# Kernel optimization log

Hardware: AMD Instinct MI355X
Metric: run time of the kernel (lower is better)

Reference implementation:

```python
import jax, jax.numpy as jnp
from jax import lax
import numpy as np

T, IN, H, L = 8192, 128, 1024, 3


def setup_inputs() -> dict:
    key = jax.random.key(0)
    ks = jax.random.split(key, 12)
    s = 0.05  # scale params to avoid saturating sigmoid/tanh
    return {
        "S": jax.random.normal(ks[0], (T, IN), jnp.float32),
        "h0": jax.random.normal(ks[1], (L, H), jnp.float32),
        "w_ih0": jax.random.normal(ks[2], (2 * H, IN), jnp.float32) * s,
        "w_hh0": jax.random.normal(ks[3], (2 * H, H), jnp.float32) * s,
        "b_ih0": jax.random.normal(ks[4], (2 * H,), jnp.float32) * s,
        "b_hh0": jax.random.normal(ks[5], (2 * H,), jnp.float32) * s,
        "w_ih_rest": jax.random.normal(ks[6], (L - 1, 2 * H, H), jnp.float32) * s,
        "w_hh_rest": jax.random.normal(ks[7], (L - 1, 2 * H, H), jnp.float32) * s,
        "b_ih_rest": jax.random.normal(ks[8], (L - 1, 2 * H), jnp.float32) * s,
        "b_hh_rest": jax.random.normal(ks[9], (L - 1, 2 * H), jnp.float32) * s,
        "w_out": jax.random.normal(ks[10], (1, H), jnp.float32) * s,
        "b_out": jax.random.normal(ks[11], (1,), jnp.float32) * s,
    }


def _mgu_layer(x_seq, h0, w_ih, w_hh, b_ih, b_hh):
    # Precompute the input projection for all timesteps at once: [T, 2H]
    gi = x_seq @ w_ih.T + b_ih

    def step(h, gi_t):
        gh = h @ w_hh.T + b_hh                      # [2H]
        i_f, i_n = jnp.split(gi_t, 2)
        h_f, h_n = jnp.split(gh, 2)
        f = jax.nn.sigmoid(i_f + h_f)               # forget gate
        n = jnp.tanh(i_n + f * h_n)                 # new candidate
        hy = n + (1.0 - f) * (h - n)
        return hy, hy

    _, out = lax.scan(step, h0, gi)                 # out: [T, H]
    return out


def reference(S, h0, w_ih0, w_hh0, b_ih0, b_hh0,
              w_ih_rest, w_hh_rest, b_ih_rest, b_hh_rest,
              w_out, b_out):
    x = _mgu_layer(S, h0[0], w_ih0, w_hh0, b_ih0, b_hh0)
    for l in range(w_ih_rest.shape[0]):             # fixed small layer count
        x = _mgu_layer(x, h0[l + 1], w_ih_rest[l], w_hh_rest[l],
                       b_ih_rest[l], b_hh_rest[l])
    out = (x @ w_out.T + b_out).reshape(-1)          # [T]
    return out
```

## Files before the change

### kernel.cpp

```cpp
#include <hip/hip_runtime.h>
#include <math.h>
#include <stdint.h>


#define T_STEPS 8192
#define HDIM 1024
#define RING 128

typedef unsigned long long u64;
typedef int v4i __attribute__((ext_vector_type(4)));

__device__ __forceinline__ u64 agload64(const u64* p) {
    return __hip_atomic_load(p, __ATOMIC_RELAXED, __HIP_MEMORY_SCOPE_AGENT);
}
__device__ __forceinline__ void agstore64(u64* p, u64 v) {
    __hip_atomic_store(p, v, __ATOMIC_RELAXED, __HIP_MEMORY_SCOPE_AGENT);
}
__device__ __forceinline__ int agloadi(const int* p) {
    return __hip_atomic_load(p, __ATOMIC_RELAXED, __HIP_MEMORY_SCOPE_AGENT);
}
__device__ __forceinline__ void agstorei(int* p, int v) {
    __hip_atomic_store(p, v, __ATOMIC_RELAXED, __HIP_MEMORY_SCOPE_AGENT);
}
__device__ __forceinline__ v4i poll16(const u64* p) {
    v4i r;
    asm volatile("global_load_dwordx4 %0, %1, off sc0 sc1\n\t"
                 "s_waitcnt vmcnt(0)"
                 : "=v"(r) : "v"(p) : "memory");
    return r;
}
__device__ __forceinline__ float dot4(float4 a, float4 b) {
    return a.x * b.x + a.y * b.y + a.z * b.z + a.w * b.w;
}
__device__ __forceinline__ u64 pack(float v, int tag) {
    return ((u64)(unsigned)tag << 32) | (u64)__float_as_uint(v);
}
__device__ __forceinline__ void opaque4(float4& v) {
    asm volatile("" : "+v"(v.x), "+v"(v.y), "+v"(v.z), "+v"(v.w));
}
__device__ __forceinline__ void opaque2(float2& v) {
    asm volatile("" : "+v"(v.x), "+v"(v.y));
}

template <int K, int L>
__device__ void scan_layer(float* __restrict__ s_h,
                           float* __restrict__ s_x,
                           const float* __restrict__ S,
                           const u64*  __restrict__ xring_in,
                           u64*        __restrict__ xring_out,
                           float*      __restrict__ xout,
                           const float* __restrict__ h0,
                           const float* __restrict__ w_ih,
                           const float* __restrict__ b_ih,
                           const float* __restrict__ w_hh,
                           const float* __restrict__ b_hh,
                           u64* __restrict__ htag,
                           int* __restrict__ progNext,
                           int* __restrict__ progSelf,
                           int r)
{
    const int tid = threadIdx.x;
    const int a   = tid >> 6;
    const int q   = tid & 63;
    const int jb  = r * 16 + 2 * a;

    float4 wf[2][4], wn[2][4];
#pragma unroll
    for (int g = 0; g < 2; ++g) {
        const float* rf = w_hh + (size_t)(jb + g) * HDIM;
        const float* rn = w_hh + (size_t)(HDIM + jb + g) * HDIM;
#pragma unroll
        for (int m = 0; m < 4; ++m) {
            wf[g][m] = *(const float4*)(rf + 4 * q + 256 * m);
            wn[g][m] = *(const float4*)(rn + 4 * q + 256 * m);
            opaque4(wf[g][m]); opaque4(wn[g][m]);
        }
    }
    float4 wif[2][4], win[2][4];
    float2 wif2[2], win2[2];
    if constexpr (K == 1024) {
#pragma unroll
        for (int g = 0; g < 2; ++g) {
            const float* rf = w_ih + (size_t)(jb + g) * K;
            const float* rn = w_ih + (size_t)(HDIM + jb + g) * K;
#pragma unroll
            for (int m = 0; m < 4; ++m) {
                wif[g][m] = *(const float4*)(rf + 4 * q + 256 * m);
                win[g][m] = *(const float4*)(rn + 4 * q + 256 * m);
                opaque4(wif[g][m]); opaque4(win[g][m]);
            }
        }
    } else {
#pragma unroll
        for (int g = 0; g < 2; ++g) {
            wif2[g] = *(const float2*)(w_ih + (size_t)(jb + g) * K + 2 * q);
            win2[g] = *(const float2*)(w_ih + (size_t)(HDIM + jb + g) * K + 2 * q);
            opaque2(wif2[g]); opaque2(win2[g]);
        }
    }
    float bFv[2], bInv[2], bHnv[2];
#pragma unroll
    for (int g = 0; g < 2; ++g) {
        bFv[g]  = b_ih[jb + g] + b_hh[jb + g];
        bInv[g] = b_ih[HDIM + jb + g];
        bHnv[g] = b_hh[HDIM + jb + g];
    }

    int lastProg = 0;
    for (int t = 0; t < T_STEPS; ++t) {
        const int par = t & 1;
        const u64* hrow = htag + (size_t)((t + 1) & 1) * HDIM;
        u64*       hpub = htag + (size_t)par * HDIM;
        float* hD = s_h + par * HDIM;
        float* xD = s_x + par * HDIM;

        if constexpr (L < 2) {
            if (t - lastProg > RING - 16) {
                do { lastProg = agloadi(progNext); } while (t - lastProg > RING - 16);
            }
        }

        if constexpr (L > 0) {
            const u64* xrow = xring_in + (size_t)(t & (RING - 1)) * HDIM;
            const unsigned xe = (unsigned)(t + 1);
            for (;;) {
                const v4i v = poll16(xrow + 2 * tid);
                if ((unsigned)v.y == xe && (unsigned)v.w == xe) {
                    ((float2*)xD)[tid] =
                        make_float2(__int_as_float(v.x), __int_as_float(v.z));
                    break;
                }
                __builtin_amdgcn_s_sleep(1);
            }
        } else {
            if (tid < K / 4)
                ((float4*)xD)[tid] = ((const float4*)(S + (size_t)t * K))[tid];
        }

        if (t == 0) {
            ((float2*)hD)[tid] = ((const float2*)h0)[tid];
        } else {
            const unsigned he = (unsigned)t;
            for (;;) {
                const v4i v = poll16(hrow + 2 * tid);
                if ((unsigned)v.y == he && (unsigned)v.w == he) {
                    ((float2*)hD)[tid] =
                        make_float2(__int_as_float(v.x), __int_as_float(v.z));
                    break;
                }
                __builtin_amdgcn_s_sleep(1);
            }
        }
        __syncthreads();

        if constexpr (L > 0) {
            if (r == 0 && tid == 0) agstorei(progSelf, t + 1);
        }

        float aF[2]  = {0.f, 0.f};
        float aNh[2] = {0.f, 0.f};
        float aNi[2] = {0.f, 0.f};
#pragma unroll
        for (int m = 0; m < 4; ++m) {
            const float4 h4 = ((const float4*)hD)[q + 64 * m];
#pragma unroll
            for (int g = 0; g < 2; ++g) {
                aF[g]  += dot4(wf[g][m], h4);
                aNh[g] += dot4(wn[g][m], h4);
            }
        }
        if constexpr (K == 1024) {
#pragma unroll
            for (int m = 0; m < 4; ++m) {
                const float4 x4 = ((const float4*)xD)[q + 64 * m];
#pragma unroll
                for (int g = 0; g < 2; ++g) {
                    aF[g]  += dot4(wif[g][m], x4);
                    aNi[g] += dot4(win[g][m], x4);
                }
            }
        } else {
            const float2 x2 = *(const float2*)&xD[2 * q];
#pragma unroll
            for (int g = 0; g < 2; ++g) {
                aF[g]  += wif2[g].x * x2.x + wif2[g].y * x2.y;
                aNi[g] += win2[g].x * x2.x + win2[g].y * x2.y;
            }
        }

#pragma unroll
        for (int g = 0; g < 2; ++g) {
            aF[g]  += __shfl_xor(aF[g],  1, 64);
            aNh[g] += __shfl_xor(aNh[g], 1, 64);
            aNi[g] += __shfl_xor(aNi[g], 1, 64);
        }
        const int gs = q & 1;
        float vF  = gs ? aF[1]  : aF[0];
        float vNh = gs ? aNh[1] : aNh[0];
        float vNi = gs ? aNi[1] : aNi[0];
#pragma unroll
        for (int off = 2; off <= 32; off <<= 1) {
            vF  += __shfl_xor(vF,  off, 64);
            vNh += __shfl_xor(vNh, off, 64);
            vNi += __shfl_xor(vNi, off, 64);
        }

        if (q < 2) {
            const float cF  = gs ? bFv[1]  : bFv[0];
            const float cIn = gs ? bInv[1] : bInv[0];
            const float cHn = gs ? bHnv[1] : bHnv[0];
            const int   j   = jb + q;
            const float hp  = hD[j];
            const float f   = 1.f / (1.f + expf(-(vF + cF)));
            const float n   = tanhf(vNi + cIn + f * (vNh + cHn));
            const float hy  = n + (1.f - f) * (hp - n);
            const u64   pk  = pack(hy, t + 1);
            agstore64(hpub + j, pk);
            if constexpr (L < 2) {
                agstore64(xring_out + (size_t)(t & (RING - 1)) * HDIM + j, pk);
            } else {
                xout[(size_t)t * HDIM + j] = hy;
            }
        }
    }
}

__global__ __launch_bounds__(512, 2)
void mgu_pipe(const float* __restrict__ S,
              const float* __restrict__ h0,
              const float* __restrict__ w_ih0, const float* __restrict__ b_ih0,
              const float* __restrict__ w_hh0, const float* __restrict__ b_hh0,
              const float* __restrict__ w_ih_r, const float* __restrict__ b_ih_r,
              const float* __restrict__ w_hh_r, const float* __restrict__ b_hh_r,
              float* __restrict__ xbuf2, u64* __restrict__ ring0,
              u64* __restrict__ ring1, u64* __restrict__ htag,
              int* __restrict__ prog)
{
    __shared__ __align__(16) float s_h[2 * HDIM];
    __shared__ __align__(16) float s_x[2 * HDIM];
    const int grp = blockIdx.x >> 6;
    const int r   = blockIdx.x & 63;
    if (grp == 0) {
        scan_layer<128, 0>(s_h, s_x, S, nullptr, ring0, nullptr, h0,
                           w_ih0, b_ih0, w_hh0, b_hh0,
                           htag, prog + 1, nullptr, r);
    } else if (grp == 1) {
        scan_layer<1024, 1>(s_h, s_x, nullptr, ring0, ring1, nullptr, h0 + HDIM,
                            w_ih_r, b_ih_r, w_hh_r, b_hh_r,
                            htag + 2 * HDIM, prog + 2, prog + 1, r);
    } else {
        scan_layer<1024, 2>(s_h, s_x, nullptr, ring1, nullptr, xbuf2,
                            h0 + 2 * HDIM,
                            w_ih_r + 2048 * 1024, b_ih_r + 2048,
                            w_hh_r + 2048 * 1024, b_hh_r + 2048,
                            htag + 4 * HDIM, nullptr, prog + 2, r);
    }
}

__global__ __launch_bounds__(256)
void mgu_out(const float* __restrict__ x,
             const float* __restrict__ w_out,
             const float* __restrict__ b_out,
             float* __restrict__ out)
{
    const int wave = threadIdx.x >> 6;
    const int lane = threadIdx.x & 63;
    const int t = blockIdx.x * 4 + wave;
    float acc = 0.f;
#pragma unroll
    for (int m = 0; m < 4; ++m) {
        const int i4 = lane + 64 * m;
        const float4 x4 = ((const float4*)(x + (size_t)t * HDIM))[i4];
        const float4 w4 = ((const float4*)w_out)[i4];
        acc += dot4(x4, w4);
    }
#pragma unroll
    for (int off = 32; off > 0; off >>= 1) acc += __shfl_xor(acc, off, 64);
    if (lane == 0) out[t] = acc + b_out[0];
}

extern "C" void kernel_launch(void* const* d_in, const int* in_sizes, int n_in,
                              void* d_out, int out_size, void* d_ws, size_t ws_size,
                              hipStream_t stream) {
    const float* S      = (const float*)d_in[0];
    const float* h0     = (const float*)d_in[1];
    const float* w_ih0  = (const float*)d_in[2];
    const float* w_hh0  = (const float*)d_in[3];
    const float* b_ih0  = (const float*)d_in[4];
    const float* b_hh0  = (const float*)d_in[5];
    const float* w_ih_r = (const float*)d_in[6];
    const float* w_hh_r = (const float*)d_in[7];
    const float* b_ih_r = (const float*)d_in[8];
    const float* b_hh_r = (const float*)d_in[9];
    const float* w_out  = (const float*)d_in[10];
    const float* b_out  = (const float*)d_in[11];
    float* out = (float*)d_out;

    char* ws = (char*)d_ws;
    float* xbuf2 = (float*)(ws);
    u64*   ring0 = (u64*)(ws + (32u << 20));
    u64*   ring1 = (u64*)(ws + (33u << 20));
    u64*   htag  = (u64*)(ws + (34u << 20));
    int*   prog  = (int*)(ws + (34u << 20) + (64u << 10));

    mgu_pipe<<<192, 512, 0, stream>>>(S, h0, w_ih0, b_ih0, w_hh0, b_hh0,
                                      w_ih_r, b_ih_r, w_hh_r, b_hh_r,
                                      xbuf2, ring0, ring1, htag, prog);
    mgu_out<<<2048, 256, 0, stream>>>(xbuf2, w_out, b_out, out);
}
```

Baseline: 25.11 ms.

## Pin each MGU layer to one XCD, store input weights as bf16 in LDS

Each layer's 32 blocks are now mapped to a single XCD through blockIdx&7, so the per-step hidden-state exchange stays in one L2 and can be polled with L2-scope loads, with a device-coherent load every fourth poll. Each block now owns 32 hidden units instead of 16, and w_ih for layers 1 and 2 is converted to bf16 and kept in 128KB of LDS, since it no longer fits in registers. The h and x polls are merged into one loop. The risks are lower precision in the input projection, lower occupancy from the large LDS footprint, twice the compute per block on the serial critical path, and reliance on round-robin block-to-XCD placement, which is not guaranteed.

```diff
diff --git a/kernel.cpp b/kernel.cpp
--- a/kernel.cpp
+++ b/kernel.cpp
@@ -22,13 +22,34 @@
 __device__ __forceinline__ void agstorei(int* p, int v) {
     __hip_atomic_store(p, v, __ATOMIC_RELAXED, __HIP_MEMORY_SCOPE_AGENT);
 }
-__device__ __forceinline__ v4i poll16(const u64* p) {
+__device__ __forceinline__ v4i poll1_l2(const u64* p) {
+    v4i r;
+    asm volatile("global_load_dwordx4 %0, %1, off sc0\n\t"
+                 "s_waitcnt vmcnt(0)"
+                 : "=v"(r) : "v"(p) : "memory");
+    return r;
+}
+__device__ __forceinline__ v4i poll1_mall(const u64* p) {
     v4i r;
     asm volatile("global_load_dwordx4 %0, %1, off sc0 sc1\n\t"
                  "s_waitcnt vmcnt(0)"
                  : "=v"(r) : "v"(p) : "memory");
     return r;
 }
+__device__ __forceinline__ void poll2_lm(const u64* hp, const u64* xp,
+                                         v4i& h4, v4i& x4) {
+    asm volatile("global_load_dwordx4 %0, %2, off sc0\n\t"
+                 "global_load_dwordx4 %1, %3, off sc0 sc1\n\t"
+                 "s_waitcnt vmcnt(0)"
+                 : "=&v"(h4), "=&v"(x4) : "v"(hp), "v"(xp) : "memory");
+}
+__device__ __forceinline__ void poll2_mm(const u64* hp, const u64* xp,
+                                         v4i& h4, v4i& x4) {
+    asm volatile("global_load_dwordx4 %0, %2, off sc0 sc1\n\t"
+                 "global_load_dwordx4 %1, %3, off sc0 sc1\n\t"
+                 "s_waitcnt vmcnt(0)"
+                 : "=&v"(h4), "=&v"(x4) : "v"(hp), "v"(xp) : "memory");
+}
 __device__ __forceinline__ float dot4(float4 a, float4 b) {
     return a.x * b.x + a.y * b.y + a.z * b.z + a.w * b.w;
 }
@@ -40,11 +61,25 @@
 }
 __device__ __forceinline__ void opaque2(float2& v) {
     asm volatile("" : "+v"(v.x), "+v"(v.y));
+}
+__device__ __forceinline__ float sel4(float a0, float a1, float a2, float a3, int g) {
+    const float t01 = (g & 1) ? a1 : a0;
+    const float t23 = (g & 1) ? a3 : a2;
+    return (g & 2) ? t23 : t01;
+}
+__device__ __forceinline__ unsigned short f2bf(float f) {
+    unsigned u = __float_as_uint(f);
+    return (unsigned short)((u + 0x7fffu + ((u >> 16) & 1u)) >> 16);
+}
+__device__ __forceinline__ void fma2(float& acc, unsigned w, float x0, float x1) {
+    acc += __uint_as_float(w << 16) * x0;
+    acc += __uint_as_float(w & 0xffff0000u) * x1;
 }
 
 template <int K, int L>
 __device__ void scan_layer(float* __restrict__ s_h,
                            float* __restrict__ s_x,
+                           unsigned* __restrict__ s_wih,
                            const float* __restrict__ S,
                            const u64*  __restrict__ xring_in,
                            u64*        __restrict__ xring_out,
@@ -57,16 +92,33 @@
                            u64* __restrict__ htag,
                            int* __restrict__ progNext,
                            int* __restrict__ progSelf,
-                           int r)
+                           int slot)
 {
     const int tid = threadIdx.x;
     const int a   = tid >> 6;
     const int q   = tid & 63;
-    const int jb  = r * 16 + 2 * a;
-
-    float4 wf[2][4], wn[2][4];
-#pragma unroll
-    for (int g = 0; g < 2; ++g) {
+    const int jb  = slot * 32 + 4 * a;
+
+    if constexpr (K == 1024) {
+        const int base = slot * 32;
+#pragma unroll 4
+        for (int it = 0; it < 64; ++it) {
+            const int flat  = tid + 512 * it;
+            const int rowid = flat >> 9;
+            const int rem   = flat & 511;
+            const int qq    = rem >> 3;
+            const int d     = rem & 7;
+            const int e     = 256 * (d >> 1) + 4 * qq + 2 * (d & 1);
+            const int grow  = (rowid < 32) ? (base + rowid)
+                                           : (HDIM + base + rowid - 32);
+            const float2 v = *(const float2*)(w_ih + (size_t)grow * K + e);
+            s_wih[flat] = (unsigned)f2bf(v.x) | ((unsigned)f2bf(v.y) << 16);
+        }
+    }
+
+    float4 wf[4][4], wn[4][4];
+#pragma unroll
+    for (int g = 0; g < 4; ++g) {
         const float* rf = w_hh + (size_t)(jb + g) * HDIM;
         const float* rn = w_hh + (size_t)(HDIM + jb + g) * HDIM;
 #pragma unroll
@@ -76,35 +128,23 @@
             opaque4(wf[g][m]); opaque4(wn[g][m]);
         }
     }
-    float4 wif[2][4], win[2][4];
-    float2 wif2[2], win2[2];
-    if constexpr (K == 1024) {
-#pragma unroll
-        for (int g = 0; g < 2; ++g) {
-            const float* rf = w_ih + (size_t)(jb + g) * K;
-            const float* rn = w_ih + (size_t)(HDIM + jb + g) * K;
-#pragma unroll
-            for (int m = 0; m < 4; ++m) {
-                wif[g][m] = *(const float4*)(rf + 4 * q + 256 * m);
-                win[g][m] = *(const float4*)(rn + 4 * q + 256 * m);
-                opaque4(wif[g][m]); opaque4(win[g][m]);
-            }
-        }
-    } else {
-#pragma unroll
-        for (int g = 0; g < 2; ++g) {
+    float2 wif2[4], win2[4];
+    if constexpr (K == 128) {
+#pragma unroll
+        for (int g = 0; g < 4; ++g) {
             wif2[g] = *(const float2*)(w_ih + (size_t)(jb + g) * K + 2 * q);
             win2[g] = *(const float2*)(w_ih + (size_t)(HDIM + jb + g) * K + 2 * q);
             opaque2(wif2[g]); opaque2(win2[g]);
         }
     }
-    float bFv[2], bInv[2], bHnv[2];
-#pragma unroll
-    for (int g = 0; g < 2; ++g) {
+    float bFv[4], bInv[4], bHnv[4];
+#pragma unroll
+    for (int g = 0; g < 4; ++g) {
         bFv[g]  = b_ih[jb + g] + b_hh[jb + g];
         bInv[g] = b_ih[HDIM + jb + g];
         bHnv[g] = b_hh[HDIM + jb + g];
     }
+    __syncthreads();
 
     int lastProg = 0;
     for (int t = 0; t < T_STEPS; ++t) {
@@ -120,95 +160,125 @@
             }
         }
 
-        if constexpr (L > 0) {
-            const u64* xrow = xring_in + (size_t)(t & (RING - 1)) * HDIM;
-            const unsigned xe = (unsigned)(t + 1);
-            for (;;) {
-                const v4i v = poll16(xrow + 2 * tid);
-                if ((unsigned)v.y == xe && (unsigned)v.w == xe) {
-                    ((float2*)xD)[tid] =
-                        make_float2(__int_as_float(v.x), __int_as_float(v.z));
-                    break;
-                }
-                __builtin_amdgcn_s_sleep(1);
-            }
-        } else {
+        bool hd = (t == 0);
+        bool xd = (L == 0);
+        if (t == 0) ((float2*)hD)[tid] = ((const float2*)h0)[tid];
+        if constexpr (L == 0) {
             if (tid < K / 4)
                 ((float4*)xD)[tid] = ((const float4*)(S + (size_t)t * K))[tid];
         }
-
-        if (t == 0) {
-            ((float2*)hD)[tid] = ((const float2*)h0)[tid];
+        {
+            const u64* hp = hrow + 2 * tid;
+            const u64* xp = (L > 0)
+                ? xring_in + (size_t)(t & (RING - 1)) * HDIM + 2 * tid : nullptr;
+            const unsigned he = (unsigned)t;
+            const unsigned xe = (unsigned)(t + 1);
+            float2 hv2 = make_float2(0.f, 0.f), xv2 = make_float2(0.f, 0.f);
+            v4i A = {0, 0, 0, 0}, B = {0, 0, 0, 0};
+            int it = 0;
+            while (!(hd && xd)) {
+                const bool mall = ((it & 3) == 3);
+                if (!hd && !xd) {
+                    if (mall) poll2_mm(hp, xp, A, B); else poll2_lm(hp, xp, A, B);
+                } else if (!hd) {
+                    A = mall ? poll1_mall(hp) : poll1_l2(hp);
+                } else {
+                    B = poll1_mall(xp);
+                }
+                if (!hd && (unsigned)A.y == he && (unsigned)A.w == he) {
+                    hv2 = make_float2(__int_as_float(A.x), __int_as_float(A.z));
+                    hd = true;
+                }
+                if (L > 0 && !xd && (unsigned)B.y == xe && (unsigned)B.w == xe) {
+                    xv2 = make_float2(__int_as_float(B.x), __int_as_float(B.z));
+                    xd = true;
+                }
+                ++it;
+            }
+            if (t > 0) ((float2*)hD)[tid] = hv2;
+            if constexpr (L > 0) ((float2*)xD)[tid] = xv2;
+        }
+        __syncthreads();
+
+        if constexpr (L > 0) {
+            if (slot == 0 && tid == 0) agstorei(progSelf, t + 1);
+        }
+
+        float4 hq[4];
+#pragma unroll
+        for (int m = 0; m < 4; ++m) hq[m] = ((const float4*)hD)[q + 64 * m];
+
+        float aF[4]  = {0.f, 0.f, 0.f, 0.f};
+        float aNh[4] = {0.f, 0.f, 0.f, 0.f};
+        float aNi[4] = {0.f, 0.f, 0.f, 0.f};
+#pragma unroll
+        for (int m = 0; m < 4; ++m) {
+#pragma unroll
+            for (int g = 0; g < 4; ++g) {
+                aF[g]  += dot4(wf[g][m], hq[m]);
+                aNh[g] += dot4(wn[g][m], hq[m]);
+            }
+        }
+        if constexpr (K == 1024) {
+            float4 xq[4];
+#pragma unroll
+            for (int m = 0; m < 4; ++m) xq[m] = ((const float4*)xD)[q + 64 * m];
+#pragma unroll
+            for (int g = 0; g < 4; ++g) {
+                const int u = 4 * a + g;
+                const unsigned* wrF = &s_wih[(size_t)(u * 64 + q) * 8];
+                const unsigned* wrN = &s_wih[(size_t)((32 + u) * 64 + q) * 8];
+                const uint4 F0 = *(const uint4*)wrF;
+                const uint4 F1 = *(const uint4*)(wrF + 4);
+                const uint4 N0 = *(const uint4*)wrN;
+                const uint4 N1 = *(const uint4*)(wrN + 4);
+                fma2(aF[g], F0.x, xq[0].x, xq[0].y);
+                fma2(aF[g], F0.y, xq[0].z, xq[0].w);
+                fma2(aF[g], F0.z, xq[1].x, xq[1].y);
+                fma2(aF[g], F0.w, xq[1].z, xq[1].w);
+                fma2(aF[g], F1.x, xq[2].x, xq[2].y);
+                fma2(aF[g], F1.y, xq[2].z, xq[2].w);
+                fma2(aF[g], F1.z, xq[3].x, xq[3].y);
+                fma2(aF[g], F1.w, xq[3].z, xq[3].w);
+                fma2(aNi[g], N0.x, xq[0].x, xq[0].y);
+                fma2(aNi[g], N0.y, xq[0].z, xq[0].w);
+                fma2(aNi[g], N0.z, xq[1].x, xq[1].y);
+                fma2(aNi[g], N0.w, xq[1].z, xq[1].w);
+                fma2(aNi[g], N1.x, xq[2].x, xq[2].y);
+                fma2(aNi[g], N1.y, xq[2].z, xq[2].w);
+                fma2(aNi[g], N1.z, xq[3].x, xq[3].y);
+                fma2(aNi[g], N1.w, xq[3].z, xq[3].w);
+            }
         } else {
-            const unsigned he = (unsigned)t;
-            for (;;) {
-                const v4i v = poll16(hrow + 2 * tid);
-                if ((unsigned)v.y == he && (unsigned)v.w == he) {
-                    ((float2*)hD)[tid] =
-                        make_float2(__int_as_float(v.x), __int_as_float(v.z));
-                    break;
-                }
-                __builtin_amdgcn_s_sleep(1);
-            }
-        }
-        __syncthreads();
-
-        if constexpr (L > 0) {
-            if (r == 0 && tid == 0) agstorei(progSelf, t + 1);
-        }
-
-        float aF[2]  = {0.f, 0.f};
-        float aNh[2] = {0.f, 0.f};
-        float aNi[2] = {0.f, 0.f};
-#pragma unroll
-        for (int m = 0; m < 4; ++m) {
-            const float4 h4 = ((const float4*)hD)[q + 64 * m];
-#pragma unroll
-            for (int g = 0; g < 2; ++g) {
-                aF[g]  += dot4(wf[g][m], h4);
-                aNh[g] += dot4(wn[g][m], h4);
-            }
-        }
-        if constexpr (K == 1024) {
-#pragma unroll
-            for (int m = 0; m < 4; ++m) {
-                const float4 x4 = ((const float4*)xD)[q + 64 * m];
-#pragma unroll
-                for (int g = 0; g < 2; ++g) {
-                    aF[g]  += dot4(wif[g][m], x4);
-                    aNi[g] += dot4(win[g][m], x4);
-                }
-            }
-        } else {
-            const float2 x2 = *(const float2*)&xD[2 * q];
-#pragma unroll
-            for (int g = 0; g < 2; ++g) {
+            const float2 x2 = ((const float2*)xD)[q];
+#pragma unroll
+            for (int g = 0; g < 4; ++g) {
                 aF[g]  += wif2[g].x * x2.x + wif2[g].y * x2.y;
                 aNi[g] += win2[g].x * x2.x + win2[g].y * x2.y;
             }
         }
 
 #pragma unroll
-        for (int g = 0; g < 2; ++g) {
-            aF[g]  += __shfl_xor(aF[g],  1, 64);
-            aNh[g] += __shfl_xor(aNh[g], 1, 64);
-            aNi[g] += __shfl_xor(aNi[g], 1, 64);
-        }
-        const int gs = q & 1;
-        float vF  = gs ? aF[1]  : aF[0];
-        float vNh = gs ? aNh[1] : aNh[0];
-        float vNi = gs ? aNi[1] : aNi[0];
-#pragma unroll
-        for (int off = 2; off <= 32; off <<= 1) {
+        for (int g = 0; g < 4; ++g) {
+            aF[g]  += __shfl_xor(aF[g], 1, 64);  aF[g]  += __shfl_xor(aF[g], 2, 64);
+            aNh[g] += __shfl_xor(aNh[g], 1, 64); aNh[g] += __shfl_xor(aNh[g], 2, 64);
+            aNi[g] += __shfl_xor(aNi[g], 1, 64); aNi[g] += __shfl_xor(aNi[g], 2, 64);
+        }
+        const int gs = q & 3;
+        float vF  = sel4(aF[0],  aF[1],  aF[2],  aF[3],  gs);
+        float vNh = sel4(aNh[0], aNh[1], aNh[2], aNh[3], gs);
+        float vNi = sel4(aNi[0], aNi[1], aNi[2], aNi[3], gs);
+#pragma unroll
+        for (int off = 4; off <= 32; off <<= 1) {
             vF  += __shfl_xor(vF,  off, 64);
             vNh += __shfl_xor(vNh, off, 64);
             vNi += __shfl_xor(vNi, off, 64);
         }
 
-        if (q < 2) {
-            const float cF  = gs ? bFv[1]  : bFv[0];
-            const float cIn = gs ? bInv[1] : bInv[0];
-            const float cHn = gs ? bHnv[1] : bHnv[0];
+        if (q < 4) {
+            const float cF  = sel4(bFv[0],  bFv[1],  bFv[2],  bFv[3],  q);
+            const float cIn = sel4(bInv[0], bInv[1], bInv[2], bInv[3], q);
+            const float cHn = sel4(bHnv[0], bHnv[1], bHnv[2], bHnv[3], q);
             const int   j   = jb + q;
             const float hp  = hD[j];
             const float f   = 1.f / (1.f + expf(-(vF + cF)));
@@ -236,24 +306,25 @@
               u64* __restrict__ ring1, u64* __restrict__ htag,
               int* __restrict__ prog)
 {
-    __shared__ __align__(16) float s_h[2 * HDIM];
-    __shared__ __align__(16) float s_x[2 * HDIM];
-    const int grp = blockIdx.x >> 6;
-    const int r   = blockIdx.x & 63;
-    if (grp == 0) {
-        scan_layer<128, 0>(s_h, s_x, S, nullptr, ring0, nullptr, h0,
+    __shared__ __align__(16) float    s_h[2 * HDIM];
+    __shared__ __align__(16) float    s_x[2 * HDIM];
+    __shared__ __align__(16) unsigned s_wih[64 * 512];
+    const int xcd  = blockIdx.x & 7;
+    const int slot = blockIdx.x >> 3;
+    if (xcd == 0) {
+        scan_layer<128, 0>(s_h, s_x, s_wih, S, nullptr, ring0, nullptr, h0,
                            w_ih0, b_ih0, w_hh0, b_hh0,
-                           htag, prog + 1, nullptr, r);
-    } else if (grp == 1) {
-        scan_layer<1024, 1>(s_h, s_x, nullptr, ring0, ring1, nullptr, h0 + HDIM,
-                            w_ih_r, b_ih_r, w_hh_r, b_hh_r,
-                            htag + 2 * HDIM, prog + 2, prog + 1, r);
-    } else {
-        scan_layer<1024, 2>(s_h, s_x, nullptr, ring1, nullptr, xbuf2,
+                           htag, prog + 1, nullptr, slot);
+    } else if (xcd == 1) {
+        scan_layer<1024, 1>(s_h, s_x, s_wih, nullptr, ring0, ring1, nullptr,
+                            h0 + HDIM, w_ih_r, b_ih_r, w_hh_r, b_hh_r,
+                            htag + 2 * HDIM, prog + 2, prog + 1, slot);
+    } else if (xcd == 2) {
+        scan_layer<1024, 2>(s_h, s_x, s_wih, nullptr, ring1, nullptr, xbuf2,
                             h0 + 2 * HDIM,
                             w_ih_r + 2048 * 1024, b_ih_r + 2048,
                             w_hh_r + 2048 * 1024, b_hh_r + 2048,
-                            htag + 4 * HDIM, nullptr, prog + 2, r);
+                            htag + 4 * HDIM, nullptr, prog + 2, slot);
     }
 }
 
@@ -303,7 +374,7 @@
     u64*   htag  = (u64*)(ws + (34u << 20));
     int*   prog  = (int*)(ws + (34u << 20) + (64u << 10));
 
-    mgu_pipe<<<192, 512, 0, stream>>>(S, h0, w_ih0, b_ih0, w_hh0, b_hh0,
+    mgu_pipe<<<256, 512, 0, stream>>>(S, h0, w_ih0, b_ih0, w_hh0, b_hh0,
                                       w_ih_r, b_ih_r, w_hh_r, b_hh_r,
                                       xbuf2, ring0, ring1, htag, prog);
     mgu_out<<<2048, 256, 0, stream>>>(xbuf2, w_out, b_out, out);
```

Result: slower. 45.39 ms (+80.8%).
